# Kernel tuning notes

Hardware: AMD Instinct MI355X
Metric: run time of the kernel (lower is better)

## Reference

```python
import jax, jax.numpy as jnp
import numpy as np
import math

D_MODEL = 512
D_FF = 2048
N_HEADS = 8
D_K = 64
EPS = 1e-5


def _layernorm(x, g, b):
    mu = jnp.mean(x, axis=-1, keepdims=True)
    var = jnp.mean(jnp.square(x - mu), axis=-1, keepdims=True)
    return (x - mu) * jax.lax.rsqrt(var + EPS) * g + b


def _pos_encoding(seq_len, d_model, dtype):
    pos = jnp.arange(seq_len, dtype=jnp.float32)[:, None]                 # [S,1]
    div = jnp.exp(jnp.arange(0, d_model, 2, dtype=jnp.float32) * (-math.log(10000.0) / d_model))
    ang = pos * div                                                        # [S,D/2]
    pe = jnp.stack([jnp.sin(ang), jnp.cos(ang)], axis=-1).reshape(seq_len, d_model)
    return pe.astype(dtype)


def setup_inputs() -> dict:
    key = jax.random.key(0)
    ks = jax.random.split(key, 16)
    B, S, D, F, H, DK = 4096, 16, D_MODEL, D_FF, N_HEADS, D_K
    s = lambda fan_in: 1.0 / np.sqrt(fan_in)
    u = lambda k, shp, sc: jax.random.uniform(k, shp, jnp.float32, -sc, sc)
    return {
        "enc_inputs": jax.random.normal(ks[0], (B, S, D), jnp.float32),
        # Linear weights stored as [in, out] (torch stores [out, in])
        "wq": u(ks[1], (D, H * DK), s(D)), "bq": u(ks[2], (H * DK,), s(D)),
        "wk": u(ks[3], (D, H * DK), s(D)), "bk": u(ks[4], (H * DK,), s(D)),
        "wv": u(ks[5], (D, H * DK), s(D)), "bv": u(ks[6], (H * DK,), s(D)),
        "wo": u(ks[7], (H * DK, D), s(H * DK)), "bo": u(ks[8], (D,), s(H * DK)),
        "ln1_g": jnp.ones((D,), jnp.float32), "ln1_b": jnp.zeros((D,), jnp.float32),
        "w1": u(ks[9], (D, F), s(D)), "b1": u(ks[10], (F,), s(D)),
        "w2": u(ks[11], (F, D), s(F)), "b2": u(ks[12], (D,), s(F)),
        "ln2_g": jnp.ones((D,), jnp.float32), "ln2_b": jnp.zeros((D,), jnp.float32),
        "conv_att_w": u(ks[13], (H,), s(H)),  # Conv2d(8,1,1,bias=False) == weighted head sum
    }


def reference(enc_inputs, wq, bq, wk, bk, wv, bv, wo, bo, ln1_g, ln1_b,
              w1, b1, w2, b2, ln2_g, ln2_b, conv_att_w):
    B, S, D = enc_inputs.shape
    H, DK = N_HEADS, D_K
    # positional encoding (dropout is identity in eval)
    x = enc_inputs + _pos_encoding(S, D, enc_inputs.dtype)[None, :, :]
    # multi-head self-attention
    q = (x @ wq + bq).reshape(B, S, H, DK).transpose(0, 2, 1, 3)  # [B,H,S,DK]
    k = (x @ wk + bk).reshape(B, S, H, DK).transpose(0, 2, 1, 3)
    v = (x @ wv + bv).reshape(B, S, H, DK).transpose(0, 2, 1, 3)
    scores = jnp.einsum('bhqd,bhkd->bhqk', q, k) / np.sqrt(DK)
    attn = jax.nn.softmax(scores, axis=-1)                         # [B,H,S,S]
    ctx = jnp.einsum('bhqk,bhkd->bhqd', attn, v)
    ctx = ctx.transpose(0, 2, 1, 3).reshape(B, S, H * DK)
    y = _layernorm(ctx @ wo + bo + x, ln1_g, ln1_b)
    # position-wise FFN (conv1d kernel=1 == linear)
    h = jax.nn.relu(y @ w1 + b1)
    out = _layernorm(h @ w2 + b2 + y, ln2_g, ln2_b)
    # conv_att: Conv2d(8->1, k=1, no bias) over heads
    attn_out = jnp.einsum('h,bhqk->bqk', conv_att_w, attn)
    return out, attn_out
```

## Files before the change

kernel.cpp:

```cpp
#include <hip/hip_runtime.h>
#include <hip/hip_bf16.h>

using bf16 = __hip_bfloat16;
typedef __attribute__((ext_vector_type(8))) short bf16x8;
typedef __attribute__((ext_vector_type(4))) float f32x4;

#define MFMA_BF16_16x16x32 __builtin_amdgcn_mfma_f32_16x16x32_bf16

__device__ __forceinline__ float bits2f(short b) {
  unsigned u = ((unsigned)(unsigned short)b) << 16;
  return __uint_as_float(u);
}
__device__ __forceinline__ short f2bits(float f) {
  bf16 h = __float2bfloat16(f);
  return *reinterpret_cast<short*>(&h);
}

__device__ __forceinline__ int xcd_swz(int bid, int nwg) {
  int q = nwg >> 3;
  return (bid & 7) * q + (bid >> 3);
}

__device__ __forceinline__ int bank_swz(int off) {
  return off ^ (((off >> 7) & 7) << 4);
}

__global__ void detect_kernel(const unsigned short* __restrict__ w, int* __restrict__ flag) {
  __shared__ int bad;
  if (threadIdx.x == 0) bad = 0;
  __syncthreads();
  float m = 0.f;
#pragma unroll
  for (int j = 0; j < 4; ++j)
    m = fmaxf(m, fabsf(bits2f((short)w[threadIdx.x * 4 + j])));
  if (m > 4.0f) atomicOr(&bad, 1);
  __syncthreads();
  if (threadIdx.x == 0) *flag = bad ? 1 : 0;
}

__global__ void pe_kernel(float* __restrict__ pe) {
  int s = blockIdx.x;
  int i = threadIdx.x;
  float dv = expf((float)(2 * i) * (-9.210340371976184f / 512.0f));
  float ang = (float)s * dv;
  pe[s * 512 + 2 * i]     = sinf(ang);
  pe[s * 512 + 2 * i + 1] = cosf(ang);
}

__global__ __launch_bounds__(256) void add_pe2_kernel(const void* __restrict__ enc_bf,
                                                      const void* __restrict__ enc_f32,
                                                      const float* __restrict__ pe,
                                                      bf16* __restrict__ x,
                                                      const int* __restrict__ flag) {
  size_t i = ((size_t)blockIdx.x * 256 + threadIdx.x) * 8;
  int col  = (int)(i & 511);
  int srow = (int)((i >> 9) & 15);
  float e[8];
  if (*flag) {
    const float* ef = (const float*)enc_f32 + i;
    f32x4 a = *reinterpret_cast<const f32x4*>(ef);
    f32x4 b = *reinterpret_cast<const f32x4*>(ef + 4);
#pragma unroll
    for (int j = 0; j < 4; ++j) { e[j] = a[j]; e[4 + j] = b[j]; }
  } else {
    bf16x8 ev = *reinterpret_cast<const bf16x8*>((const bf16*)enc_bf + i);
#pragma unroll
    for (int j = 0; j < 8; ++j) e[j] = bits2f(ev[j]);
  }
  const float* pp = pe + srow * 512 + col;
  f32x4 p0 = *reinterpret_cast<const f32x4*>(pp);
  f32x4 p1 = *reinterpret_cast<const f32x4*>(pp + 4);
  bf16x8 o;
#pragma unroll
  for (int j = 0; j < 4; ++j) o[j] = f2bits(e[j] + p0[j]);
#pragma unroll
  for (int j = 0; j < 4; ++j) o[4 + j] = f2bits(e[4 + j] + p1[j]);
  *reinterpret_cast<bf16x8*>(x + i) = o;
}

__global__ __launch_bounds__(256) void transpose_cvt_kernel(const void* __restrict__ src,
                                                            unsigned short* __restrict__ dst,
                                                            int R, int C, const int* __restrict__ flag) {
  __shared__ unsigned short t[32][33];
  int bx = blockIdx.x * 32;
  int by = blockIdx.y * 32;
  int lx = threadIdx.x & 31, ly = threadIdx.x >> 5;
  if (*flag) {
    const float* s = (const float*)src;
#pragma unroll
    for (int i = 0; i < 4; ++i)
      t[ly + i * 8][lx] = (unsigned short)f2bits(s[(size_t)(by + ly + i * 8) * C + bx + lx]);
  } else {
    const unsigned short* s = (const unsigned short*)src;
#pragma unroll
    for (int i = 0; i < 4; ++i)
      t[ly + i * 8][lx] = s[(size_t)(by + ly + i * 8) * C + bx + lx];
  }
  __syncthreads();
#pragma unroll
  for (int i = 0; i < 4; ++i)
    dst[(size_t)(bx + ly + i * 8) * R + by + lx] = t[lx][ly + i * 8];
}

struct SmallSeg { const void* src; bf16* dst; int n; };
struct SmallCvtArgs { SmallSeg seg[11]; };
__global__ __launch_bounds__(256) void small_cvt_kernel(SmallCvtArgs a, const int* __restrict__ flag) {
  SmallSeg s = a.seg[blockIdx.x];
  int f = *flag;
  for (int i = threadIdx.x; i < s.n; i += 256) {
    float v = f ? ((const float*)s.src)[i] : bits2f(((const short*)s.src)[i]);
    s.dst[i] = __float2bfloat16(v);
  }
}

template <int EPI>
__global__ __launch_bounds__(512, 4)
void gemm9_kernel(const bf16* __restrict__ A, const bf16* __restrict__ Bt,
                  const bf16* __restrict__ bias, const bf16* res,
                  bf16* C, int M, int N, int K) {
  __shared__ __align__(16) char lds[2][24576];
  const int nbn = N >> 7;
  const int wg = xcd_swz(blockIdx.x, gridDim.x);
  const int bn = wg % nbn, bm = wg / nbn;
  const int m0 = bm << 8, n0 = bn << 7;
  const int tid = threadIdx.x, lane = tid & 63, wid = tid >> 6;
  const int wr = wid >> 1, wc = wid & 1;
  const int lr = lane & 15, gq = lane >> 4;
  const int nt = K >> 5;

  f32x4 acc[4][4] = {};
  bf16x8 a[4], b[4];

  auto stage = [&](int s) {
    const int buf = s & 1;
#pragma unroll
    for (int l = 0; l < 2; ++l) {
      int p = l * 8192 + tid * 16;
      int q = bank_swz(p);
      const bf16* src = A + (size_t)(m0 + (q >> 6)) * K + s * 32 + ((q & 63) >> 1);
      __builtin_amdgcn_global_load_lds(
          (const __attribute__((address_space(1))) void*)src,
          (__attribute__((address_space(3))) void*)&lds[buf][l * 8192 + wid * 1024], 16, 0, 0);
    }
    {
      int p = tid * 16;
      int q = bank_swz(p);
      const bf16* src = Bt + (size_t)(n0 + (q >> 6)) * K + s * 32 + ((q & 63) >> 1);
      __builtin_amdgcn_global_load_lds(
          (const __attribute__((address_space(1))) void*)src,
          (__attribute__((address_space(3))) void*)&lds[buf][16384 + wid * 1024], 16, 0, 0);
    }
  };

  auto rdA = [&](int buf, int row) -> bf16x8 {
    int off = bank_swz(row * 64 + gq * 16);
    return *reinterpret_cast<const bf16x8*>(&lds[buf][off]);
  };
  auto rdB = [&](int buf, int row) -> bf16x8 {
    int off = bank_swz(row * 64 + gq * 16);
    return *reinterpret_cast<const bf16x8*>(&lds[buf][16384 + off]);
  };

  stage(0); stage(1);
  asm volatile("s_waitcnt vmcnt(3)" ::: "memory");
  __builtin_amdgcn_s_barrier();

  for (int s = 0; s < nt; ++s) {
    const int buf = s & 1;
#pragma unroll
    for (int mf = 0; mf < 4; ++mf) a[mf] = rdA(buf, wr * 64 + mf * 16 + lr);
#pragma unroll
    for (int nf = 0; nf < 4; ++nf) b[nf] = rdB(buf, wc * 64 + nf * 16 + lr);
    asm volatile("s_waitcnt lgkmcnt(0)" ::: "memory");
    __builtin_amdgcn_sched_barrier(0);
    __builtin_amdgcn_s_barrier();
    const bool st = (s + 2 < nt);
    if (st) stage(s + 2);
    __builtin_amdgcn_s_setprio(1);
#pragma unroll
    for (int mf = 0; mf < 4; ++mf)
#pragma unroll
      for (int nf = 0; nf < 4; ++nf)
        acc[mf][nf] = MFMA_BF16_16x16x32(a[mf], b[nf], acc[mf][nf], 0, 0, 0);
    __builtin_amdgcn_s_setprio(0);
    if (st) asm volatile("s_waitcnt vmcnt(3)" ::: "memory");
    else    asm volatile("s_waitcnt vmcnt(0)" ::: "memory");
    __builtin_amdgcn_s_barrier();
  }

#pragma unroll
  for (int mf = 0; mf < 4; ++mf) {
#pragma unroll
    for (int nf = 0; nf < 4; ++nf) {
      int col = n0 + wc * 64 + nf * 16 + lr;
      float bv = __bfloat162float(bias[col]);
#pragma unroll
      for (int r = 0; r < 4; ++r) {
        int row = m0 + wr * 64 + mf * 16 + gq * 4 + r;
        float v = acc[mf][nf][r] + bv;
        if (EPI == 1) v = fmaxf(v, 0.0f);
        if (EPI == 2) v += __bfloat162float(res[(size_t)row * N + col]);
        C[(size_t)row * N + col] = __float2bfloat16(v);
      }
    }
  }
}

__global__ __launch_bounds__(256)
void attn_kernel(const bf16* __restrict__ qkv, const bf16* __restrict__ cw,
                 bf16* __restrict__ ctx, float* __restrict__ attn_out) {
  __shared__ __align__(16) unsigned short qkv_lds[16][1544];
  __shared__ __align__(16) unsigned short p_lds[4][16][16];
  __shared__ float att_lds[4][16][16];
  const int b = blockIdx.x;
  const int tid = threadIdx.x, lane = tid & 63, w = tid >> 6;
  const int lr = lane & 15, g = lane >> 4;
  const bf16* src = qkv + (size_t)b * 16 * 1536;
  for (int t = tid; t < 16 * 192; t += 256) {
    int row = t / 192, ch = t - row * 192;
    *reinterpret_cast<bf16x8*>(&qkv_lds[row][ch * 8]) =
        *reinterpret_cast<const bf16x8*>(src + (size_t)row * 1536 + ch * 8);
  }
  __syncthreads();
  float attacc[4] = {0.f, 0.f, 0.f, 0.f};

  for (int hh = 0; hh < 2; ++hh) {
    const int h = w * 2 + hh;
    const unsigned short* qp = &qkv_lds[lr][h * 64 + g * 8];
    const unsigned short* kp = qp + 512;
    bf16x8 q0 = *reinterpret_cast<const bf16x8*>(qp);
    bf16x8 q1 = *reinterpret_cast<const bf16x8*>(qp + 32);
    bf16x8 k0 = *reinterpret_cast<const bf16x8*>(kp);
    bf16x8 k1 = *reinterpret_cast<const bf16x8*>(kp + 32);
    f32x4 s = {0.f, 0.f, 0.f, 0.f};
    s = MFMA_BF16_16x16x32(q0, k0, s, 0, 0, 0);
    s = MFMA_BF16_16x16x32(q1, k1, s, 0, 0, 0);
    float wgt = __bfloat162float(cw[h]);
    float p[4];
#pragma unroll
    for (int r = 0; r < 4; ++r) {
      float sv = s[r] * 0.125f;
      float mx = sv;
#pragma unroll
      for (int mm = 1; mm < 16; mm <<= 1) mx = fmaxf(mx, __shfl_xor(mx, mm, 16));
      float e = expf(sv - mx);
      float sm = e;
#pragma unroll
      for (int mm = 1; mm < 16; mm <<= 1) sm += __shfl_xor(sm, mm, 16);
      p[r] = e / sm;
      attacc[r] += wgt * p[r];
    }
#pragma unroll
    for (int r = 0; r < 4; ++r) p_lds[w][g * 4 + r][lr] = (unsigned short)f2bits(p[r]);
    __syncthreads();
    bf16x8 pa;
#pragma unroll
    for (int j = 0; j < 8; ++j) pa[j] = 0;
    if (g < 2) pa = *reinterpret_cast<const bf16x8*>(&p_lds[w][lr][g * 8]);
#pragma unroll
    for (int n = 0; n < 4; ++n) {
      bf16x8 vb;
#pragma unroll
      for (int j = 0; j < 8; ++j) vb[j] = 0;
      if (g < 2) {
#pragma unroll
        for (int j = 0; j < 8; ++j)
          vb[j] = (short)qkv_lds[g * 8 + j][1024 + h * 64 + n * 16 + lr];
      }
      f32x4 z = {0.f, 0.f, 0.f, 0.f};
      f32x4 d = MFMA_BF16_16x16x32(pa, vb, z, 0, 0, 0);
#pragma unroll
      for (int r = 0; r < 4; ++r)
        ctx[(size_t)(b * 16 + g * 4 + r) * 512 + h * 64 + n * 16 + lr] = __float2bfloat16(d[r]);
    }
    __syncthreads();
  }
#pragma unroll
  for (int r = 0; r < 4; ++r) att_lds[w][g * 4 + r][lr] = attacc[r];
  __syncthreads();
  const int q = tid >> 4, kk = tid & 15;
  float ssum = att_lds[0][q][kk] + att_lds[1][q][kk] + att_lds[2][q][kk] + att_lds[3][q][kk];
  attn_out[(size_t)b * 256 + q * 16 + kk] = ssum;
}

template <int F32OUT>
__global__ __launch_bounds__(256, 4)
void ln_kernel(const bf16* in, const bf16* __restrict__ gw,
               const bf16* __restrict__ bw, void* out) {
  const int row = blockIdx.x * 4 + (threadIdx.x >> 6);
  const int lane = threadIdx.x & 63;
  const bf16* rp = in + (size_t)row * 512 + lane * 8;
  bf16x8 xv = *reinterpret_cast<const bf16x8*>(rp);
  float xf[8];
#pragma unroll
  for (int j = 0; j < 8; ++j) xf[j] = bits2f(xv[j]);
  float s = 0.f;
#pragma unroll
  for (int j = 0; j < 8; ++j) s += xf[j];
#pragma unroll
  for (int o = 32; o >= 1; o >>= 1) s += __shfl_xor(s, o, 64);
  float mu = s * (1.0f / 512.0f);
  float v = 0.f;
#pragma unroll
  for (int j = 0; j < 8; ++j) { float d = xf[j] - mu; v += d * d; }
#pragma unroll
  for (int o = 32; o >= 1; o >>= 1) v += __shfl_xor(v, o, 64);
  float rs = rsqrtf(v * (1.0f / 512.0f) + 1e-5f);
  bf16x8 gv = *reinterpret_cast<const bf16x8*>(gw + lane * 8);
  bf16x8 bv = *reinterpret_cast<const bf16x8*>(bw + lane * 8);
  if (F32OUT) {
    float* op = (float*)out + (size_t)row * 512 + lane * 8;
    f32x4 o0, o1;
#pragma unroll
    for (int j = 0; j < 4; ++j) {
      o0[j] = (xf[j] - mu) * rs * bits2f(gv[j]) + bits2f(bv[j]);
      o1[j] = (xf[4 + j] - mu) * rs * bits2f(gv[4 + j]) + bits2f(bv[4 + j]);
    }
    *reinterpret_cast<f32x4*>(op) = o0;
    *reinterpret_cast<f32x4*>(op + 4) = o1;
  } else {
    bf16x8 o8;
#pragma unroll
    for (int j = 0; j < 8; ++j)
      o8[j] = f2bits((xf[j] - mu) * rs * bits2f(gv[j]) + bits2f(bv[j]));
    *reinterpret_cast<bf16x8*>((bf16*)out + (size_t)row * 512 + lane * 8) = o8;
  }
}

extern "C" void kernel_launch(void* const* d_in, const int* in_sizes, int n_in,
                              void* d_out, int out_size, void* d_ws, size_t ws_size,
                              hipStream_t stream) {
  const void* enc  = d_in[0];
  const void* wq   = d_in[1];
  const void* bq   = d_in[2];
  const void* wk   = d_in[3];
  const void* bk   = d_in[4];
  const void* wv   = d_in[5];
  const void* bvv  = d_in[6];
  const void* wo   = d_in[7];
  const void* bo   = d_in[8];
  const void* ln1g = d_in[9];
  const void* ln1b = d_in[10];
  const void* w1   = d_in[11];
  const void* b1   = d_in[12];
  const void* w2   = d_in[13];
  const void* b2   = d_in[14];
  const void* ln2g = d_in[15];
  const void* ln2b = d_in[16];
  const void* cw   = d_in[17];

  float* outp     = (float*)d_out;
  float* attn_out = outp + (size_t)33554432;

  char* wsp = (char*)d_ws;
  size_t off = 0;
  auto alloc = [&](size_t bytes) {
    void* p = wsp + off;
    off = (off + bytes + 255) & ~(size_t)255;
    return p;
  };
  int*  flag  = (int*)alloc(4);
  float* pe   = (float*)alloc((size_t)16 * 512 * 4);
  bf16* wqkvT = (bf16*)alloc((size_t)1536 * 512 * 2);
  bf16* woT   = (bf16*)alloc((size_t)512 * 512 * 2);
  bf16* w1T   = (bf16*)alloc((size_t)2048 * 512 * 2);
  bf16* w2T   = (bf16*)alloc((size_t)512 * 2048 * 2);
  bf16* bqkv  = (bf16*)alloc((size_t)1536 * 2);
  bf16* bo_c  = (bf16*)alloc((size_t)512 * 2);
  bf16* b1_c  = (bf16*)alloc((size_t)2048 * 2);
  bf16* b2_c  = (bf16*)alloc((size_t)512 * 2);
  bf16* l1g_c = (bf16*)alloc((size_t)512 * 2);
  bf16* l1b_c = (bf16*)alloc((size_t)512 * 2);
  bf16* l2g_c = (bf16*)alloc((size_t)512 * 2);
  bf16* l2b_c = (bf16*)alloc((size_t)512 * 2);
  bf16* cw_c  = (bf16*)alloc((size_t)8 * 2);
  size_t fixed_bytes = off;

  int CH = 1024;
  {
    const int cands[6] = {65536, 32768, 16384, 8192, 4096, 2048};
    for (int ci = 0; ci < 6; ++ci) {
      size_t need = fixed_bytes + (size_t)cands[ci] * 6144 + (1u << 20);
      if (need <= ws_size) { CH = cands[ci]; break; }
    }
  }
  bf16* x_c   = (bf16*)alloc((size_t)CH * 512 * 2);
  bf16* ctx_c = (bf16*)alloc((size_t)CH * 512 * 2);
  bf16* share = (bf16*)alloc((size_t)CH * 2048 * 2);
  bf16* qkv = share;
  bf16* h   = share;
  bf16* y_c = ctx_c;

  detect_kernel<<<1, 256, 0, stream>>>((const unsigned short*)wq, flag);
  pe_kernel<<<16, 256, 0, stream>>>(pe);
  transpose_cvt_kernel<<<dim3(16, 16), 256, 0, stream>>>(wq, (unsigned short*)wqkvT, 512, 512, flag);
  transpose_cvt_kernel<<<dim3(16, 16), 256, 0, stream>>>(wk, (unsigned short*)(wqkvT + 512 * 512), 512, 512, flag);
  transpose_cvt_kernel<<<dim3(16, 16), 256, 0, stream>>>(wv, (unsigned short*)(wqkvT + 1024 * 512), 512, 512, flag);
  transpose_cvt_kernel<<<dim3(16, 16), 256, 0, stream>>>(wo, (unsigned short*)woT, 512, 512, flag);
  transpose_cvt_kernel<<<dim3(64, 16), 256, 0, stream>>>(w1, (unsigned short*)w1T, 512, 2048, flag);
  transpose_cvt_kernel<<<dim3(16, 64), 256, 0, stream>>>(w2, (unsigned short*)w2T, 2048, 512, flag);
  {
    SmallCvtArgs a;
    a.seg[0]  = {bq,   bqkv,        512};
    a.seg[1]  = {bk,   bqkv + 512,  512};
    a.seg[2]  = {bvv,  bqkv + 1024, 512};
    a.seg[3]  = {bo,   bo_c,        512};
    a.seg[4]  = {b1,   b1_c,       2048};
    a.seg[5]  = {b2,   b2_c,        512};
    a.seg[6]  = {ln1g, l1g_c,       512};
    a.seg[7]  = {ln1b, l1b_c,       512};
    a.seg[8]  = {ln2g, l2g_c,       512};
    a.seg[9]  = {ln2b, l2b_c,       512};
    a.seg[10] = {cw,   cw_c,          8};
    small_cvt_kernel<<<11, 256, 0, stream>>>(a, flag);
  }

  for (int r0 = 0; r0 < 65536; r0 += CH) {
    float* out_c = outp + (size_t)r0 * 512;
    float* ao_c  = attn_out + (size_t)(r0 / 16) * 256;
    add_pe2_kernel<<<CH / 4, 256, 0, stream>>>(
        (const void*)((const bf16*)enc + (size_t)r0 * 512),
        (const void*)((const float*)enc + (size_t)r0 * 512), pe, x_c, flag);
    gemm9_kernel<0><<<(CH / 256) * 12, 512, 0, stream>>>(x_c, wqkvT, bqkv, nullptr, qkv, CH, 1536, 512);
    attn_kernel<<<CH / 16, 256, 0, stream>>>(qkv, cw_c, ctx_c, ao_c);
    gemm9_kernel<2><<<(CH / 256) * 4, 512, 0, stream>>>(ctx_c, woT, bo_c, x_c, x_c, CH, 512, 512);
    ln_kernel<0><<<CH / 4, 256, 0, stream>>>(x_c, l1g_c, l1b_c, y_c);
    gemm9_kernel<1><<<(CH / 256) * 16, 512, 0, stream>>>(y_c, w1T, b1_c, nullptr, h, CH, 2048, 512);
    gemm9_kernel<2><<<(CH / 256) * 4, 512, 0, stream>>>(h, w2T, b2_c, y_c, y_c, CH, 512, 2048);
    ln_kernel<1><<<CH / 4, 256, 0, stream>>>(y_c, l2g_c, l2b_c, out_c);
  }
}
```

Baseline: 804.2 us.

## Fuse output-projection and FFN2 GEMMs with residual add and LayerNorm

Adds a GEMM kernel whose 64-row tile spans the full 512-wide output, so each workgroup can finish the bias, the residual add and the LayerNorm in its epilogue through a cross-wave LDS reduction of sum and sum of squares. This removes two separate LayerNorm launches and the round trip of the pre-norm activations through global memory. In exchange the tiles are narrower in M (64 instead of 256), so B-matrix reuse per workgroup falls and each workgroup streams the whole weight matrix. Variance is now computed as E[x²]−mu² on fp32 values before bf16 rounding, which changes numerics slightly.

Result: slower. 842.3 us (+4.7%).

```diff
diff --git a/kernel.cpp b/kernel.cpp
--- a/kernel.cpp
+++ b/kernel.cpp
@@ -206,6 +206,143 @@
   }
 }
 
+template <int F32OUT>
+__global__ __launch_bounds__(512, 4)
+void gemm_ln_kernel(const bf16* __restrict__ A, const bf16* __restrict__ Bt,
+                    const bf16* __restrict__ bias, const bf16* __restrict__ res,
+                    const bf16* __restrict__ gw, const bf16* __restrict__ bw,
+                    void* __restrict__ Cout, int M, int K) {
+  __shared__ __align__(16) char ldsA[2][4096];
+  __shared__ __align__(16) char ldsB[2][32768];
+  const int wg = xcd_swz(blockIdx.x, gridDim.x);
+  const int m0 = wg << 6;
+  const int tid = threadIdx.x, lane = tid & 63, w = tid >> 6;
+  const int lr = lane & 15, gq = lane >> 4;
+  const int nt = K >> 5;
+
+  f32x4 acc[4][4] = {};
+  bf16x8 a[4], b[4];
+
+  auto stage = [&](int s) {
+    const int buf = s & 1;
+    {
+      int p = (w & 3) * 1024 + lane * 16;
+      int q = bank_swz(p);
+      const bf16* src = A + (size_t)(m0 + (q >> 6)) * K + s * 32 + ((q & 63) >> 1);
+      __builtin_amdgcn_global_load_lds(
+          (const __attribute__((address_space(1))) void*)src,
+          (__attribute__((address_space(3))) void*)&ldsA[buf][(w & 3) * 1024], 16, 0, 0);
+    }
+#pragma unroll
+    for (int l = 0; l < 4; ++l) {
+      int p = l * 8192 + w * 1024 + lane * 16;
+      int q = bank_swz(p);
+      const bf16* src = Bt + (size_t)(q >> 6) * K + s * 32 + ((q & 63) >> 1);
+      __builtin_amdgcn_global_load_lds(
+          (const __attribute__((address_space(1))) void*)src,
+          (__attribute__((address_space(3))) void*)&ldsB[buf][l * 8192 + w * 1024], 16, 0, 0);
+    }
+  };
+
+  auto rdA = [&](int buf, int row) -> bf16x8 {
+    int off = bank_swz(row * 64 + gq * 16);
+    return *reinterpret_cast<const bf16x8*>(&ldsA[buf][off]);
+  };
+  auto rdB = [&](int buf, int row) -> bf16x8 {
+    int off = bank_swz(row * 64 + gq * 16);
+    return *reinterpret_cast<const bf16x8*>(&ldsB[buf][off]);
+  };
+
+  stage(0); stage(1);
+  asm volatile("s_waitcnt vmcnt(5)" ::: "memory");
+  __builtin_amdgcn_s_barrier();
+
+  for (int s = 0; s < nt; ++s) {
+    const int buf = s & 1;
+#pragma unroll
+    for (int mf = 0; mf < 4; ++mf) a[mf] = rdA(buf, mf * 16 + lr);
+#pragma unroll
+    for (int nf = 0; nf < 4; ++nf) b[nf] = rdB(buf, w * 64 + nf * 16 + lr);
+    asm volatile("s_waitcnt lgkmcnt(0)" ::: "memory");
+    __builtin_amdgcn_sched_barrier(0);
+    __builtin_amdgcn_s_barrier();
+    const bool st = (s + 2 < nt);
+    if (st) stage(s + 2);
+    __builtin_amdgcn_s_setprio(1);
+#pragma unroll
+    for (int mf = 0; mf < 4; ++mf)
+#pragma unroll
+      for (int nf = 0; nf < 4; ++nf)
+        acc[mf][nf] = MFMA_BF16_16x16x32(a[mf], b[nf], acc[mf][nf], 0, 0, 0);
+    __builtin_amdgcn_s_setprio(0);
+    if (st) asm volatile("s_waitcnt vmcnt(5)" ::: "memory");
+    else    asm volatile("s_waitcnt vmcnt(0)" ::: "memory");
+    __builtin_amdgcn_s_barrier();
+  }
+
+  float bsv[4], gvv[4], bwv[4];
+  int col[4];
+#pragma unroll
+  for (int nf = 0; nf < 4; ++nf) {
+    col[nf] = w * 64 + nf * 16 + lr;
+    bsv[nf] = __bfloat162float(bias[col[nf]]);
+    gvv[nf] = __bfloat162float(gw[col[nf]]);
+    bwv[nf] = __bfloat162float(bw[col[nf]]);
+  }
+#pragma unroll
+  for (int mf = 0; mf < 4; ++mf)
+#pragma unroll
+    for (int rr = 0; rr < 4; ++rr) {
+      int rowg = m0 + mf * 16 + gq * 4 + rr;
+#pragma unroll
+      for (int nf = 0; nf < 4; ++nf)
+        acc[mf][nf][rr] += bsv[nf] + __bfloat162float(res[(size_t)rowg * 512 + col[nf]]);
+    }
+  float* redS = (float*)&ldsB[0][0];
+  float* redQ = (float*)&ldsB[0][2048];
+#pragma unroll
+  for (int mf = 0; mf < 4; ++mf)
+#pragma unroll
+    for (int rr = 0; rr < 4; ++rr) {
+      float s1 = 0.f, s2 = 0.f;
+#pragma unroll
+      for (int nf = 0; nf < 4; ++nf) { float v = acc[mf][nf][rr]; s1 += v; s2 += v * v; }
+#pragma unroll
+      for (int mm = 1; mm < 16; mm <<= 1) {
+        s1 += __shfl_xor(s1, mm, 16);
+        s2 += __shfl_xor(s2, mm, 16);
+      }
+      if (lr == 0) {
+        int rowl = mf * 16 + gq * 4 + rr;
+        redS[rowl * 8 + w] = s1;
+        redQ[rowl * 8 + w] = s2;
+      }
+    }
+  __syncthreads();
+#pragma unroll
+  for (int mf = 0; mf < 4; ++mf)
+#pragma unroll
+    for (int rr = 0; rr < 4; ++rr) {
+      int rowl = mf * 16 + gq * 4 + rr;
+      f32x4 sa = *reinterpret_cast<f32x4*>(&redS[rowl * 8]);
+      f32x4 sb = *reinterpret_cast<f32x4*>(&redS[rowl * 8 + 4]);
+      f32x4 qa = *reinterpret_cast<f32x4*>(&redQ[rowl * 8]);
+      f32x4 qb = *reinterpret_cast<f32x4*>(&redQ[rowl * 8 + 4]);
+      float S = (sa[0] + sa[1]) + (sa[2] + sa[3]) + (sb[0] + sb[1]) + (sb[2] + sb[3]);
+      float Q = (qa[0] + qa[1]) + (qa[2] + qa[3]) + (qb[0] + qb[1]) + (qb[2] + qb[3]);
+      float mu = S * (1.0f / 512.0f);
+      float var = Q * (1.0f / 512.0f) - mu * mu;
+      float rs = rsqrtf(var + 1e-5f);
+      int rowg = m0 + rowl;
+#pragma unroll
+      for (int nf = 0; nf < 4; ++nf) {
+        float o = (acc[mf][nf][rr] - mu) * rs * gvv[nf] + bwv[nf];
+        if (F32OUT) ((float*)Cout)[(size_t)rowg * 512 + col[nf]] = o;
+        else        ((bf16*)Cout)[(size_t)rowg * 512 + col[nf]] = __float2bfloat16(o);
+      }
+    }
+}
+
 __global__ __launch_bounds__(256)
 void attn_kernel(const bf16* __restrict__ qkv, const bf16* __restrict__ cw,
                  bf16* __restrict__ ctx, float* __restrict__ attn_out) {
@@ -281,50 +418,6 @@
   const int q = tid >> 4, kk = tid & 15;
   float ssum = att_lds[0][q][kk] + att_lds[1][q][kk] + att_lds[2][q][kk] + att_lds[3][q][kk];
   attn_out[(size_t)b * 256 + q * 16 + kk] = ssum;
-}
-
-template <int F32OUT>
-__global__ __launch_bounds__(256, 4)
-void ln_kernel(const bf16* in, const bf16* __restrict__ gw,
-               const bf16* __restrict__ bw, void* out) {
-  const int row = blockIdx.x * 4 + (threadIdx.x >> 6);
-  const int lane = threadIdx.x & 63;
-  const bf16* rp = in + (size_t)row * 512 + lane * 8;
-  bf16x8 xv = *reinterpret_cast<const bf16x8*>(rp);
-  float xf[8];
-#pragma unroll
-  for (int j = 0; j < 8; ++j) xf[j] = bits2f(xv[j]);
-  float s = 0.f;
-#pragma unroll
-  for (int j = 0; j < 8; ++j) s += xf[j];
-#pragma unroll
-  for (int o = 32; o >= 1; o >>= 1) s += __shfl_xor(s, o, 64);
-  float mu = s * (1.0f / 512.0f);
-  float v = 0.f;
-#pragma unroll
-  for (int j = 0; j < 8; ++j) { float d = xf[j] - mu; v += d * d; }
-#pragma unroll
-  for (int o = 32; o >= 1; o >>= 1) v += __shfl_xor(v, o, 64);
-  float rs = rsqrtf(v * (1.0f / 512.0f) + 1e-5f);
-  bf16x8 gv = *reinterpret_cast<const bf16x8*>(gw + lane * 8);
-  bf16x8 bv = *reinterpret_cast<const bf16x8*>(bw + lane * 8);
-  if (F32OUT) {
-    float* op = (float*)out + (size_t)row * 512 + lane * 8;
-    f32x4 o0, o1;
-#pragma unroll
-    for (int j = 0; j < 4; ++j) {
-      o0[j] = (xf[j] - mu) * rs * bits2f(gv[j]) + bits2f(bv[j]);
-      o1[j] = (xf[4 + j] - mu) * rs * bits2f(gv[4 + j]) + bits2f(bv[4 + j]);
-    }
-    *reinterpret_cast<f32x4*>(op) = o0;
-    *reinterpret_cast<f32x4*>(op + 4) = o1;
-  } else {
-    bf16x8 o8;
-#pragma unroll
-    for (int j = 0; j < 8; ++j)
-      o8[j] = f2bits((xf[j] - mu) * rs * bits2f(gv[j]) + bits2f(bv[j]));
-    *reinterpret_cast<bf16x8*>((bf16*)out + (size_t)row * 512 + lane * 8) = o8;
-  }
 }
 
 extern "C" void kernel_launch(void* const* d_in, const int* in_sizes, int n_in,
@@ -423,10 +516,8 @@
         (const void*)((const float*)enc + (size_t)r0 * 512), pe, x_c, flag);
     gemm9_kernel<0><<<(CH / 256) * 12, 512, 0, stream>>>(x_c, wqkvT, bqkv, nullptr, qkv, CH, 1536, 512);
     attn_kernel<<<CH / 16, 256, 0, stream>>>(qkv, cw_c, ctx_c, ao_c);
-    gemm9_kernel<2><<<(CH / 256) * 4, 512, 0, stream>>>(ctx_c, woT, bo_c, x_c, x_c, CH, 512, 512);
-    ln_kernel<0><<<CH / 4, 256, 0, stream>>>(x_c, l1g_c, l1b_c, y_c);
+    gemm_ln_kernel<0><<<CH / 64, 512, 0, stream>>>(ctx_c, woT, bo_c, x_c, l1g_c, l1b_c, y_c, CH, 512);
     gemm9_kernel<1><<<(CH / 256) * 16, 512, 0, stream>>>(y_c, w1T, b1_c, nullptr, h, CH, 2048, 512);
-    gemm9_kernel<2><<<(CH / 256) * 4, 512, 0, stream>>>(h, w2T, b2_c, y_c, y_c, CH, 512, 2048);
-    ln_kernel<1><<<CH / 4, 256, 0, stream>>>(y_c, l2g_c, l2b_c, out_c);
-  }
-}
+    gemm_ln_kernel<1><<<CH / 64, 512, 0, stream>>>(h, w2T, b2_c, y_c, l2g_c, l2b_c, out_c, CH, 2048);
+  }
+}
```
